# Optimization experiments

Measured on AMD Instinct MI355X. Metric: run time of the kernel, lower is better.

The kernel has to match this reference:

```python
import jax, jax.numpy as jnp
import numpy as np

B, S, D = 4, 1024, 1024
H, DK, DV = 16, 64, 64
LN_EPS = 1e-5

def setup_inputs() -> dict:
    key = jax.random.key(0)
    ks = jax.random.split(key, 8)
    sc_q = 1.0 / np.sqrt(D)
    return {
        "Q": jax.random.normal(ks[0], (B, S, D), jnp.float32),
        "K": jax.random.normal(ks[1], (B, S, D), jnp.float32),
        "V": jax.random.normal(ks[2], (B, S, D), jnp.float32),
        "mask": jnp.zeros((B, S, S), dtype=bool),
        "W_Q": jax.random.normal(ks[3], (D, H * DK), jnp.float32) * sc_q,
        "W_K": jax.random.normal(ks[4], (D, H * DK), jnp.float32) * sc_q,
        "W_V": jax.random.normal(ks[5], (D, H * DV), jnp.float32) * sc_q,
        "W_O": jax.random.normal(ks[6], (H * DV, D), jnp.float32) * (1.0 / np.sqrt(H * DV)),
        "ln_gamma": jnp.ones((D,), jnp.float32),
        "ln_beta": jnp.zeros((D,), jnp.float32),
    }

def reference(Q, K, V, mask, W_Q, W_K, W_V, W_O, ln_gamma, ln_beta):
    residual = Q
    # projections -> [B, H, S, dk/dv]
    q = (Q @ W_Q).reshape(B, S, H, DK).transpose(0, 2, 1, 3)
    k = (K @ W_K).reshape(B, S, H, DK).transpose(0, 2, 1, 3)
    v = (V @ W_V).reshape(B, S, H, DV).transpose(0, 2, 1, 3)
    # scores [B, H, Sq, Sk]
    scores = jnp.einsum('bhqd,bhkd->bhqk', q, k) / jnp.sqrt(jnp.float32(DK))
    scores = jnp.where(mask[:, None, :, :], -jnp.inf, scores)
    # faithful to original: softmax over dim=2 (the QUERY axis)
    attn = jax.nn.softmax(scores, axis=2)
    out = jnp.einsum('bhqk,bhkd->bhqd', attn, v)  # [B, H, Sq, dv]
    out = out.transpose(0, 2, 1, 3).reshape(B, S, H * DV)
    out = out @ W_O + residual
    # LayerNorm over last dim
    mu = jnp.mean(out, axis=-1, keepdims=True)
    var = jnp.var(out, axis=-1, keepdims=True)
    out = (out - mu) * jax.lax.rsqrt(var + LN_EPS) * ln_gamma + ln_beta
    return out, attn
```

## Files before the change

### kernel.cpp

```cpp
#include <hip/hip_runtime.h>
#include <hip/hip_bf16.h>


typedef __bf16 bf16;
typedef bf16 bf16x4 __attribute__((ext_vector_type(4)));
typedef bf16 bf16x8 __attribute__((ext_vector_type(8)));
typedef float f32x4 __attribute__((ext_vector_type(4)));
typedef unsigned char u8x16 __attribute__((ext_vector_type(16)));

#define MFMA(a, b, c) __builtin_amdgcn_mfma_f32_16x16x32_bf16((a), (b), (c), 0, 0, 0)

__device__ __forceinline__ bf16 f2b(float x) { return (bf16)x; }

__device__ __forceinline__ void gl_lds16(const bf16* g, void* l) {
    __builtin_amdgcn_global_load_lds(
        (const __attribute__((address_space(1))) void*)g,
        (__attribute__((address_space(3))) void*)l, 16, 0, 0);
}

__device__ __forceinline__ void wait_lgkm() {
    __builtin_amdgcn_sched_barrier(0);
    asm volatile("s_waitcnt lgkmcnt(0)" ::: "memory");
    __builtin_amdgcn_sched_barrier(0);
}

__device__ __forceinline__ void bar_only() {
    __builtin_amdgcn_sched_barrier(0);
    __builtin_amdgcn_s_barrier();
    __builtin_amdgcn_sched_barrier(0);
}

__device__ __forceinline__ void bar_lgkm() {
    wait_lgkm();
    bar_only();
}

__global__ __launch_bounds__(256) void k_cvt(
    const float* __restrict__ Q, const float* __restrict__ K, const float* __restrict__ V,
    bf16* __restrict__ Qb, bf16* __restrict__ Kb, bf16* __restrict__ Vb)
{
    const int z = blockIdx.y;
    const float* src = z == 0 ? Q : z == 1 ? K : V;
    bf16* dst = z == 0 ? Qb : z == 1 ? Kb : Vb;
    const float sc = z == 0 ? 0.125f : 1.0f;
    size_t idx = ((size_t)blockIdx.x * 256 + threadIdx.x) * 8;
    const size_t stride = (size_t)gridDim.x * 2048;
    for (; idx < 4194304; idx += stride) {
        const float4 v0 = *(const float4*)(src + idx);
        const float4 v1 = *(const float4*)(src + idx + 4);
        bf16x8 o = { f2b(v0.x * sc), f2b(v0.y * sc), f2b(v0.z * sc), f2b(v0.w * sc),
                     f2b(v1.x * sc), f2b(v1.y * sc), f2b(v1.z * sc), f2b(v1.w * sc) };
        *(bf16x8*)(dst + idx) = o;
    }
}

__global__ __launch_bounds__(256) void k_transpose(
    const float* __restrict__ W0, const float* __restrict__ W1,
    const float* __restrict__ W2, const float* __restrict__ W3,
    bf16* __restrict__ T0, bf16* __restrict__ T1,
    bf16* __restrict__ T2, bf16* __restrict__ T3)
{
    const float* W = blockIdx.z == 0 ? W0 : blockIdx.z == 1 ? W1 : blockIdx.z == 2 ? W2 : W3;
    bf16*        T = blockIdx.z == 0 ? T0 : blockIdx.z == 1 ? T1 : blockIdx.z == 2 ? T2 : T3;
    __shared__ float tile[32][33];
    const int t = threadIdx.x;
    const int r = t >> 3, c = (t & 7) * 4;
    {
        const float4 v = *(const float4*)(W + (size_t)(blockIdx.y * 32 + r) * 1024 + blockIdx.x * 32 + c);
        tile[r][c + 0] = v.x; tile[r][c + 1] = v.y; tile[r][c + 2] = v.z; tile[r][c + 3] = v.w;
    }
    __syncthreads();
    bf16x4 o = { f2b(tile[c + 0][r]), f2b(tile[c + 1][r]), f2b(tile[c + 2][r]), f2b(tile[c + 3][r]) };
    *(bf16x4*)(T + (size_t)(blockIdx.x * 32 + r) * 1024 + blockIdx.y * 32 + c) = o;
}

__global__ __launch_bounds__(256) void k_proj(
    const bf16* __restrict__ Xq, const bf16* __restrict__ Xk, const bf16* __restrict__ Xv,
    const bf16* __restrict__ WTq, const bf16* __restrict__ WTk, const bf16* __restrict__ WTv,
    bf16* __restrict__ qh, bf16* __restrict__ kh, bf16* __restrict__ vTh)
{
    const int z = blockIdx.z;
    const bf16* X  = z == 0 ? Xq : z == 1 ? Xk : Xv;
    const bf16* WT = z == 0 ? WTq : z == 1 ? WTk : WTv;

    __shared__ char AsB[8192];
    __shared__ char BsB[16384];

    const int tid = threadIdx.x;
    const int lane = tid & 63, w = tid >> 6;
    const int lr = lane & 15, lg = lane >> 4;
    const int wm = w >> 1, wn = w & 1;
    const int m0 = blockIdx.y * 64, n0 = blockIdx.x * 128;

    const int lrow = lane >> 3;
    const int swz8 = ((lane & 7) ^ lrow) * 8;
    const bf16* Ab = X  + (size_t)(m0 + w * 8 + lrow) * 1024 + swz8;
    const bf16* Bb = WT + (size_t)(n0 + w * 8 + lrow) * 1024 + swz8;
    char* Alb = AsB + w * 1024;
    char* Blb = BsB + w * 1024;

    f32x4 acc[2][4] = {};

    for (int k0 = 0; k0 < 1024; k0 += 64) {
        gl_lds16(Ab + k0,          Alb);
        gl_lds16(Ab + 32768 + k0,  Alb + 4096);
        #pragma unroll
        for (int i = 0; i < 4; ++i)
            gl_lds16(Bb + (size_t)i * 32768 + k0, Blb + i * 4096);
        __syncthreads();
        #pragma unroll
        for (int ks = 0; ks < 2; ++ks) {
            const int swr = ((ks * 4 + lg) ^ (lr & 7)) << 4;
            bf16x8 a[2], bb[4];
            #pragma unroll
            for (int fm = 0; fm < 2; ++fm)
                a[fm] = *(const bf16x8*)(AsB + (wm * 32 + fm * 16 + lr) * 128 + swr);
            #pragma unroll
            for (int fn = 0; fn < 4; ++fn)
                bb[fn] = *(const bf16x8*)(BsB + (wn * 64 + fn * 16 + lr) * 128 + swr);
            #pragma unroll
            for (int fm = 0; fm < 2; ++fm)
                #pragma unroll
                for (int fn = 0; fn < 4; ++fn)
                    acc[fm][fn] = MFMA(a[fm], bb[fn], acc[fm][fn]);
        }
        __syncthreads();
    }

    if (z < 2) {
        bf16* dst = (z == 0) ? qh : kh;
        #pragma unroll
        for (int fm = 0; fm < 2; ++fm)
            #pragma unroll
            for (int fn = 0; fn < 4; ++fn)
                #pragma unroll
                for (int r = 0; r < 4; ++r) {
                    const int m = m0 + wm * 32 + fm * 16 + lg * 4 + r;
                    const int n = n0 + wn * 64 + fn * 16 + lr;
                    const int b = m >> 10, s = m & 1023, h = n >> 6, d = n & 63;
                    dst[(((size_t)(b * 16 + h)) * 1024 + s) * 64 + d] = f2b(acc[fm][fn][r]);
                }
    } else {
        #pragma unroll
        for (int fm = 0; fm < 2; ++fm)
            #pragma unroll
            for (int fn = 0; fn < 4; ++fn) {
                const int m = m0 + wm * 32 + fm * 16 + lg * 4;
                const int n = n0 + wn * 64 + fn * 16 + lr;
                const int b = m >> 10, s = m & 1023, h = n >> 6, d = n & 63;
                bf16x4 o = { f2b(acc[fm][fn][0]), f2b(acc[fm][fn][1]),
                             f2b(acc[fm][fn][2]), f2b(acc[fm][fn][3]) };
                *(bf16x4*)&vTh[(((size_t)(b * 16 + h)) * 64 + d) * 1024 + s] = o;
            }
    }
}

__global__ __launch_bounds__(256) void k_colsum(
    const bf16* __restrict__ qh, const bf16* __restrict__ kh,
    const unsigned char* __restrict__ mask, float* __restrict__ inv_colsum)
{
    const int bid = blockIdx.x;
    const int wg = (bid & 7) * 256 + (bid >> 3);
    const int bh = wg >> 5;
    const int kk0 = (wg & 31) * 32;
    const int b = bh >> 4;
    const bf16* qb = qh + (size_t)bh * 65536;
    const bf16* kb = kh + (size_t)bh * 65536;
    const unsigned char* mb = mask + (size_t)b * 1048576;

    const int tid = threadIdx.x;
    const int lane = tid & 63, w = tid >> 6;
    const int lr = lane & 15, lg = lane >> 4;

    __shared__ unsigned char Ml[2][128 * 48];
    __shared__ float csum[4][32];

    const int mrow = tid >> 1, mcoff = (tid & 1) * 16;

    bf16x8 bfr[2][2];
    #pragma unroll
    for (int fn = 0; fn < 2; ++fn)
        #pragma unroll
        for (int ks = 0; ks < 2; ++ks)
            bfr[fn][ks] = *(const bf16x8*)(kb + (size_t)(kk0 + fn * 16 + lr) * 64 + ks * 32 + lg * 8);

    *(u8x16*)&Ml[0][mrow * 48 + mcoff] =
        *(const u8x16*)(mb + (size_t)mrow * 1024 + kk0 + mcoff);
    bar_lgkm();

    float colacc[2][4] = {};

    for (int q0 = 0; q0 < 1024; q0 += 128) {
        const int cur = (q0 >> 7) & 1;
        if (q0 + 128 < 1024)
            *(u8x16*)&Ml[cur ^ 1][mrow * 48 + mcoff] =
                *(const u8x16*)(mb + (size_t)(q0 + 128 + mrow) * 1024 + kk0 + mcoff);

        bf16x8 a[2][2];
        #pragma unroll
        for (int fm = 0; fm < 2; ++fm) {
            const int q = q0 + w * 32 + fm * 16 + lr;
            a[fm][0] = *(const bf16x8*)(qb + (size_t)q * 64 + lg * 8);
            a[fm][1] = *(const bf16x8*)(qb + (size_t)q * 64 + 32 + lg * 8);
        }

        #pragma unroll
        for (int fm = 0; fm < 2; ++fm) {
            const int ql = w * 32 + fm * 16 + lr;
            #pragma unroll
            for (int fn = 0; fn < 2; ++fn) {
                f32x4 c = {0.f, 0.f, 0.f, 0.f};
                c = MFMA(bfr[fn][0], a[fm][0], c);
                c = MFMA(bfr[fn][1], a[fm][1], c);
                const unsigned int m4 = *(const unsigned int*)&Ml[cur][ql * 48 + fn * 16 + lg * 4];
                #pragma unroll
                for (int r = 0; r < 4; ++r)
                    colacc[fn][r] += ((m4 >> (8 * r)) & 255u) ? 0.f : __expf(c[r]);
            }
        }
        bar_lgkm();
    }

    #pragma unroll
    for (int fn = 0; fn < 2; ++fn)
        #pragma unroll
        for (int r = 0; r < 4; ++r) {
            float v = colacc[fn][r];
            v += __shfl_xor(v, 1);
            v += __shfl_xor(v, 2);
            v += __shfl_xor(v, 4);
            v += __shfl_xor(v, 8);
            if (lr == 0) csum[w][fn * 16 + lg * 4 + r] = v;
        }
    __syncthreads();
    if (tid < 32) {
        const float s = csum[0][tid] + csum[1][tid] + csum[2][tid] + csum[3][tid];
        inv_colsum[(size_t)bh * 1024 + kk0 + tid] = 1.0f / s;
    }
}

__global__ __launch_bounds__(256) void k_attn(
    const bf16* __restrict__ qh, const bf16* __restrict__ kh, const bf16* __restrict__ vTh,
    const unsigned char* __restrict__ mask, const float* __restrict__ inv_colsum,
    float* __restrict__ attn_out, bf16* __restrict__ attn_head)
{
    const int bid = blockIdx.x;
    const int wg = (bid & 7) * 256 + (bid >> 3);
    const int bh = wg >> 5;
    const int q0 = (wg & 31) * 32;
    const int b = bh >> 4, h = bh & 15;
    const bf16* qb = qh + (size_t)bh * 65536;
    const bf16* kb = kh + (size_t)bh * 65536;
    const bf16* vb = vTh + (size_t)bh * 65536;
    const unsigned char* mb = mask + (size_t)b * 1048576 + (size_t)q0 * 1024;

    const int tid = threadIdx.x;
    const int lane = tid & 63, w = tid >> 6;
    const int lr = lane & 15, lg = lane >> 4;

    __shared__ __align__(16) char smem[17408 + 9216];
    bf16* Pl = (bf16*)smem;
    unsigned char* Ml = (unsigned char*)(smem + 17408);
    f32x4* red = (f32x4*)smem;
    bf16* Ao = (bf16*)(smem + 17408);

    const int mrow = tid >> 3, mcoff = (tid & 7) * 16;

    bf16x8 af[2][2];
    #pragma unroll
    for (int fm = 0; fm < 2; ++fm)
        #pragma unroll
        for (int ks = 0; ks < 2; ++ks)
            af[fm][ks] = *(const bf16x8*)(qb + (size_t)(q0 + fm * 16 + lr) * 64 + ks * 32 + lg * 8);

    *(u8x16*)&Ml[mrow * 144 + mcoff] = *(const u8x16*)(mb + (size_t)mrow * 1024 + mcoff);
    bar_lgkm();

    f32x4 pacc[2][4] = {};

    #pragma unroll
    for (int it = 0; it < 8; ++it) {
        const int kk0 = it << 7;
        const int cur = it & 1;
        bf16* P = Pl + cur * 32 * 136;
        const unsigned char* Mc = Ml + cur * 32 * 144;

        if (it < 7)
            *(u8x16*)&Ml[(cur ^ 1) * 4608 + mrow * 144 + mcoff] =
                *(const u8x16*)(mb + (size_t)mrow * 1024 + kk0 + 128 + mcoff);

        bf16x8 bfr[2][2];
        #pragma unroll
        for (int fn = 0; fn < 2; ++fn)
            #pragma unroll
            for (int ks = 0; ks < 2; ++ks)
                bfr[fn][ks] = *(const bf16x8*)(kb + (size_t)(kk0 + w * 32 + fn * 16 + lr) * 64 + ks * 32 + lg * 8);

        bf16x8 vv[4];
        #pragma unroll
        for (int fn2 = 0; fn2 < 4; ++fn2)
            vv[fn2] = *(const bf16x8*)(vb + (size_t)(fn2 * 16 + lr) * 1024 + kk0 + w * 32 + lg * 8);

        f32x4 linv[2];
        #pragma unroll
        for (int fn = 0; fn < 2; ++fn)
            linv[fn] = *(const f32x4*)(inv_colsum + (size_t)bh * 1024 + kk0 + w * 32 + fn * 16 + lg * 4);

        #pragma unroll
        for (int fm = 0; fm < 2; ++fm)
            #pragma unroll
            for (int fn = 0; fn < 2; ++fn) {
                f32x4 c = {0.f, 0.f, 0.f, 0.f};
                c = MFMA(bfr[fn][0], af[fm][0], c);
                c = MFMA(bfr[fn][1], af[fm][1], c);
                const int ql = fm * 16 + lr;
                const int kloc = w * 32 + fn * 16 + lg * 4;
                const unsigned int m4 = *(const unsigned int*)&Mc[ql * 144 + kloc];
                bf16x4 pb;
                #pragma unroll
                for (int r = 0; r < 4; ++r)
                    pb[r] = f2b(((m4 >> (8 * r)) & 255u) ? 0.f : __expf(c[r]) * linv[fn][r]);
                *(bf16x4*)&P[ql * 136 + kloc] = pb;
            }

        wait_lgkm();

        #pragma unroll
        for (int fm2 = 0; fm2 < 2; ++fm2) {
            const bf16x8 pa = *(const bf16x8*)&P[(fm2 * 16 + lr) * 136 + w * 32 + lg * 8];
            #pragma unroll
            for (int fn2 = 0; fn2 < 4; ++fn2)
                pacc[fm2][fn2] = MFMA(pa, vv[fn2], pacc[fm2][fn2]);
        }

        wait_lgkm();
        bar_only();

        {
            const int srow = tid >> 5;
            const int c4 = (tid & 31) * 4;
            #pragma unroll
            for (int rr = 0; rr < 4; ++rr) {
                const int row = srow + rr * 8;
                const uint2 pv = *(const uint2*)&P[row * 136 + c4];
                f32x4 o;
                o[0] = __uint_as_float(pv.x << 16);
                o[1] = __uint_as_float(pv.x & 0xffff0000u);
                o[2] = __uint_as_float(pv.y << 16);
                o[3] = __uint_as_float(pv.y & 0xffff0000u);
                *(f32x4*)(attn_out + ((size_t)bh * 1024 + q0 + row) * 1024 + kk0 + c4) = o;
            }
        }
    }

    __syncthreads();
    if (w >= 2)
        #pragma unroll
        for (int fm2 = 0; fm2 < 2; ++fm2)
            #pragma unroll
            for (int fn2 = 0; fn2 < 4; ++fn2)
                red[(fm2 * 4 + fn2) * 128 + (w - 2) * 64 + lane] = pacc[fm2][fn2];
    __syncthreads();
    if (w < 2)
        #pragma unroll
        for (int fm2 = 0; fm2 < 2; ++fm2)
            #pragma unroll
            for (int fn2 = 0; fn2 < 4; ++fn2)
                pacc[fm2][fn2] += red[(fm2 * 4 + fn2) * 128 + w * 64 + lane];
    __syncthreads();
    if (w == 1)
        #pragma unroll
        for (int fm2 = 0; fm2 < 2; ++fm2)
            #pragma unroll
            for (int fn2 = 0; fn2 < 4; ++fn2)
                red[(fm2 * 4 + fn2) * 128 + lane] = pacc[fm2][fn2];
    __syncthreads();
    if (w == 0)
        #pragma unroll
        for (int fm2 = 0; fm2 < 2; ++fm2)
            #pragma unroll
            for (int fn2 = 0; fn2 < 4; ++fn2) {
                const f32x4 s = pacc[fm2][fn2] + red[(fm2 * 4 + fn2) * 128 + lane];
                #pragma unroll
                for (int r = 0; r < 4; ++r)
                    Ao[(fm2 * 16 + lg * 4 + r) * 72 + fn2 * 16 + lr] = f2b(s[r]);
            }
    __syncthreads();
    {
        const int row = tid >> 3, c8 = (tid & 7) * 8;
        const bf16x8 v = *(const bf16x8*)&Ao[row * 72 + c8];
        *(bf16x8*)(attn_head + ((size_t)b * 1024 + q0 + row) * 1024 + h * 64 + c8) = v;
    }
}

__global__ __launch_bounds__(256) void k_outproj(
    const bf16* __restrict__ Ah, const bf16* __restrict__ WTo,
    const float* __restrict__ Qres, float* __restrict__ proj)
{
    __shared__ char AsB[8192];
    __shared__ char BsB[16384];

    const int tid = threadIdx.x;
    const int lane = tid & 63, w = tid >> 6;
    const int lr = lane & 15, lg = lane >> 4;
    const int wm = w >> 1, wn = w & 1;
    const int m0 = blockIdx.y * 64, n0 = blockIdx.x * 128;

    const int lrow = lane >> 3;
    const int swz8 = ((lane & 7) ^ lrow) * 8;
    const bf16* Ab = Ah  + (size_t)(m0 + w * 8 + lrow) * 1024 + swz8;
    const bf16* Bb = WTo + (size_t)(n0 + w * 8 + lrow) * 1024 + swz8;
    char* Alb = AsB + w * 1024;
    char* Blb = BsB + w * 1024;

    f32x4 acc[2][4] = {};

    for (int k0 = 0; k0 < 1024; k0 += 64) {
        gl_lds16(Ab + k0,         Alb);
        gl_lds16(Ab + 32768 + k0, Alb + 4096);
        #pragma unroll
        for (int i = 0; i < 4; ++i)
            gl_lds16(Bb + (size_t)i * 32768 + k0, Blb + i * 4096);
        __syncthreads();
        #pragma unroll
        for (int ks = 0; ks < 2; ++ks) {
            const int swr = ((ks * 4 + lg) ^ (lr & 7)) << 4;
            bf16x8 a[2], bb[4];
            #pragma unroll
            for (int fm = 0; fm < 2; ++fm)
                a[fm] = *(const bf16x8*)(AsB + (wm * 32 + fm * 16 + lr) * 128 + swr);
            #pragma unroll
            for (int fn = 0; fn < 4; ++fn)
                bb[fn] = *(const bf16x8*)(BsB + (wn * 64 + fn * 16 + lr) * 128 + swr);
            #pragma unroll
            for (int fm = 0; fm < 2; ++fm)
                #pragma unroll
                for (int fn = 0; fn < 4; ++fn)
                    acc[fm][fn] = MFMA(a[fm], bb[fn], acc[fm][fn]);
        }
        __syncthreads();
    }

    #pragma unroll
    for (int fm = 0; fm < 2; ++fm)
        #pragma unroll
        for (int fn = 0; fn < 4; ++fn)
            #pragma unroll
            for (int r = 0; r < 4; ++r) {
                const int m = m0 + wm * 32 + fm * 16 + lg * 4 + r;
                const int n = n0 + wn * 64 + fn * 16 + lr;
                proj[(size_t)m * 1024 + n] = acc[fm][fn][r] + Qres[(size_t)m * 1024 + n];
            }
}

__global__ __launch_bounds__(256) void k_ln(
    const float* __restrict__ proj, const float* __restrict__ gam,
    const float* __restrict__ bet, float* __restrict__ out)
{
    const int row = blockIdx.x;
    const int t = threadIdx.x;
    const int lane = t & 63, w = t >> 6;
    const float4 x = *(const float4*)(proj + (size_t)row * 1024 + t * 4);
    float s = x.x + x.y + x.z + x.w;
    float ss = x.x * x.x + x.y * x.y + x.z * x.z + x.w * x.w;
    #pragma unroll
    for (int o = 1; o < 64; o <<= 1) {
        s += __shfl_xor(s, o);
        ss += __shfl_xor(ss, o);
    }
    __shared__ float rs[4], rss[4];
    if (lane == 0) { rs[w] = s; rss[w] = ss; }
    __syncthreads();
    const float S1 = rs[0] + rs[1] + rs[2] + rs[3];
    const float S2 = rss[0] + rss[1] + rss[2] + rss[3];
    const float mu = S1 * (1.0f / 1024.0f);
    const float rstd = rsqrtf(S2 * (1.0f / 1024.0f) - mu * mu + 1e-5f);
    const float4 gg = *(const float4*)(gam + t * 4);
    const float4 bb = *(const float4*)(bet + t * 4);
    float4 y;
    y.x = (x.x - mu) * rstd * gg.x + bb.x;
    y.y = (x.y - mu) * rstd * gg.y + bb.y;
    y.z = (x.z - mu) * rstd * gg.z + bb.z;
    y.w = (x.w - mu) * rstd * gg.w + bb.w;
    *(float4*)(out + (size_t)row * 1024 + t * 4) = y;
}

extern "C" void kernel_launch(void* const* d_in, const int* in_sizes, int n_in,
                              void* d_out, int out_size, void* d_ws, size_t ws_size,
                              hipStream_t stream)
{
    const float* Q  = (const float*)d_in[0];
    const float* K  = (const float*)d_in[1];
    const float* V  = (const float*)d_in[2];
    const unsigned char* mask = (const unsigned char*)d_in[3];
    const float* W_Q = (const float*)d_in[4];
    const float* W_K = (const float*)d_in[5];
    const float* W_V = (const float*)d_in[6];
    const float* W_O = (const float*)d_in[7];
    const float* gam = (const float*)d_in[8];
    const float* bet = (const float*)d_in[9];

    float* out  = (float*)d_out;
    float* attn = out + (size_t)4 * 1024 * 1024;

    bf16* wsb = (bf16*)d_ws;
    const size_t M1 = 1024 * 1024;
    bf16* WTq = wsb + 0 * M1;
    bf16* WTk = wsb + 1 * M1;
    bf16* WTv = wsb + 2 * M1;
    bf16* WTo = wsb + 3 * M1;
    bf16* qh  = wsb + 4 * M1;
    bf16* kh  = wsb + 8 * M1;
    bf16* vTh = wsb + 12 * M1;
    bf16* Xqb = wsb + 16 * M1;
    bf16* Xkb = wsb + 20 * M1;
    bf16* Xvb = wsb + 24 * M1;
    bf16* Ah  = wsb + 16 * M1;
    float* inv_colsum = (float*)(wsb + 20 * M1);
    float* proj       = inv_colsum + 65536;

    const dim3 blk(256);
    k_cvt<<<dim3(512, 3), blk, 0, stream>>>(Q, K, V, Xqb, Xkb, Xvb);
    k_transpose<<<dim3(32, 32, 4), blk, 0, stream>>>(W_Q, W_K, W_V, W_O, WTq, WTk, WTv, WTo);
    k_proj<<<dim3(8, 64, 3), blk, 0, stream>>>(Xqb, Xkb, Xvb, WTq, WTk, WTv, qh, kh, vTh);
    k_colsum<<<dim3(2048), blk, 0, stream>>>(qh, kh, mask, inv_colsum);
    k_attn<<<dim3(2048), blk, 0, stream>>>(qh, kh, vTh, mask, inv_colsum, attn, Ah);
    k_outproj<<<dim3(8, 64), blk, 0, stream>>>(Ah, WTo, Q, proj);
    k_ln<<<dim3(4096), blk, 0, stream>>>(proj, gam, bet, out);
}
```

Before: 234.6 us.

## Make mask staging and attn writeback wave-private to drop block barriers

The attention-probability kernel now gives each wave its own slice of mask bytes in shared memory and writes back only its own 32-column strip of P to attn_out. Because no wave reads data another wave staged, the per-iteration s_barrier calls are removed and replaced by lgkmcnt waits, in both the column-sum and the output kernel. This cuts synchronisation stalls across the four waves. In exchange the attn_out stores become narrower per wave (32 columns instead of 128), and the change depends on the wave-private layout being exactly right, including the double-buffered P with no barrier between reuse.

```diff
diff --git a/kernel.cpp b/kernel.cpp
--- a/kernel.cpp
+++ b/kernel.cpp
@@ -22,17 +22,6 @@
     __builtin_amdgcn_sched_barrier(0);
     asm volatile("s_waitcnt lgkmcnt(0)" ::: "memory");
     __builtin_amdgcn_sched_barrier(0);
-}
-
-__device__ __forceinline__ void bar_only() {
-    __builtin_amdgcn_sched_barrier(0);
-    __builtin_amdgcn_s_barrier();
-    __builtin_amdgcn_sched_barrier(0);
-}
-
-__device__ __forceinline__ void bar_lgkm() {
-    wait_lgkm();
-    bar_only();
 }
 
 __global__ __launch_bounds__(256) void k_cvt(
@@ -186,7 +175,7 @@
 
     *(u8x16*)&Ml[0][mrow * 48 + mcoff] =
         *(const u8x16*)(mb + (size_t)mrow * 1024 + kk0 + mcoff);
-    bar_lgkm();
+    wait_lgkm();
 
     float colacc[2][4] = {};
 
@@ -218,7 +207,7 @@
                     colacc[fn][r] += ((m4 >> (8 * r)) & 255u) ? 0.f : __expf(c[r]);
             }
         }
-        bar_lgkm();
+        wait_lgkm();
     }
 
     #pragma unroll
@@ -258,13 +247,13 @@
     const int lane = tid & 63, w = tid >> 6;
     const int lr = lane & 15, lg = lane >> 4;
 
-    __shared__ __align__(16) char smem[17408 + 9216];
+    __shared__ __align__(16) char smem[17408 + 8192];
     bf16* Pl = (bf16*)smem;
-    unsigned char* Ml = (unsigned char*)(smem + 17408);
+    unsigned char* Mw = (unsigned char*)(smem + 17408) + w * 2048;
     f32x4* red = (f32x4*)smem;
     bf16* Ao = (bf16*)(smem + 17408);
 
-    const int mrow = tid >> 3, mcoff = (tid & 7) * 16;
+    const int msrow = lane >> 1, msoff = (lane & 1) * 16;
 
     bf16x8 af[2][2];
     #pragma unroll
@@ -273,8 +262,9 @@
         for (int ks = 0; ks < 2; ++ks)
             af[fm][ks] = *(const bf16x8*)(qb + (size_t)(q0 + fm * 16 + lr) * 64 + ks * 32 + lg * 8);
 
-    *(u8x16*)&Ml[mrow * 144 + mcoff] = *(const u8x16*)(mb + (size_t)mrow * 1024 + mcoff);
-    bar_lgkm();
+    *(u8x16*)&Mw[msrow * 32 + msoff] =
+        *(const u8x16*)(mb + (size_t)msrow * 1024 + w * 32 + msoff);
+    wait_lgkm();
 
     f32x4 pacc[2][4] = {};
 
@@ -283,11 +273,11 @@
         const int kk0 = it << 7;
         const int cur = it & 1;
         bf16* P = Pl + cur * 32 * 136;
-        const unsigned char* Mc = Ml + cur * 32 * 144;
+        const unsigned char* Mc = Mw + cur * 1024;
 
         if (it < 7)
-            *(u8x16*)&Ml[(cur ^ 1) * 4608 + mrow * 144 + mcoff] =
-                *(const u8x16*)(mb + (size_t)mrow * 1024 + kk0 + 128 + mcoff);
+            *(u8x16*)&Mw[(cur ^ 1) * 1024 + msrow * 32 + msoff] =
+                *(const u8x16*)(mb + (size_t)msrow * 1024 + kk0 + 128 + w * 32 + msoff);
 
         bf16x8 bfr[2][2];
         #pragma unroll
@@ -315,7 +305,7 @@
                 c = MFMA(bfr[fn][1], af[fm][1], c);
                 const int ql = fm * 16 + lr;
                 const int kloc = w * 32 + fn * 16 + lg * 4;
-                const unsigned int m4 = *(const unsigned int*)&Mc[ql * 144 + kloc];
+                const unsigned int m4 = *(const unsigned int*)&Mc[ql * 32 + fn * 16 + lg * 4];
                 bf16x4 pb;
                 #pragma unroll
                 for (int r = 0; r < 4; ++r)
@@ -333,22 +323,19 @@
                 pacc[fm2][fn2] = MFMA(pa, vv[fn2], pacc[fm2][fn2]);
         }
 
-        wait_lgkm();
-        bar_only();
-
         {
-            const int srow = tid >> 5;
-            const int c4 = (tid & 31) * 4;
+            const int srow = lane >> 3;
+            const int c4 = (lane & 7) * 4;
             #pragma unroll
             for (int rr = 0; rr < 4; ++rr) {
                 const int row = srow + rr * 8;
-                const uint2 pv = *(const uint2*)&P[row * 136 + c4];
+                const uint2 pv = *(const uint2*)&P[row * 136 + w * 32 + c4];
                 f32x4 o;
                 o[0] = __uint_as_float(pv.x << 16);
                 o[1] = __uint_as_float(pv.x & 0xffff0000u);
                 o[2] = __uint_as_float(pv.y << 16);
                 o[3] = __uint_as_float(pv.y & 0xffff0000u);
-                *(f32x4*)(attn_out + ((size_t)bh * 1024 + q0 + row) * 1024 + kk0 + c4) = o;
+                *(f32x4*)(attn_out + ((size_t)bh * 1024 + q0 + row) * 1024 + kk0 + w * 32 + c4) = o;
             }
         }
     }
```

Result: no change. 235.0 us (+0.2%).
